# Kernel optimization log

Measured on AMD Instinct MI355X. Metric: run time of the kernel, lower is better.

The kernel has to match this reference:

```python
import jax, jax.numpy as jnp
import numpy as np

B = 8192          # batch (parallel RL envs)
LATENT = 32       # latent_size
CIN = 128         # original input_size (obs dim), c features
HID = 256         # hidden_size
ACT = 16          # num_actions
E = 8             # num_experts
GH = 128          # gate hidden size (hardcoded in module)
IN0 = LATENT + CIN    # layer-0 input dim (160)
INTER = HID + LATENT  # layer-1/2 input dim (288)
LN_EPS = 1e-5


def setup_inputs() -> dict:
    key = jax.random.key(0)
    ks = jax.random.split(key, 10)
    s = lambda k, shape, scale=1.0: jax.random.normal(k, shape, jnp.float32) * scale
    return {
        "z": s(ks[0], (B, LATENT)),
        "c": s(ks[1], (B, CIN)),
        # expert MLP params (kaiming-like small uniform scale stand-in)
        "w0": s(ks[2], (E, IN0, HID), 0.05),   "b0": jnp.full((E, HID), 0.01, jnp.float32),
        "w1": s(ks[3], (E, INTER, HID), 0.05), "b1": jnp.full((E, HID), 0.01, jnp.float32),
        "w2": s(ks[4], (E, INTER, ACT), 0.05), "b2": jnp.full((E, ACT), 0.01, jnp.float32),
        # gate MLP params
        "g0w": s(ks[5], (IN0, GH), 0.05), "g0b": jnp.zeros((GH,), jnp.float32),
        "g1w": s(ks[6], (GH, GH), 0.05),  "g1b": jnp.zeros((GH,), jnp.float32),
        "g2w": s(ks[7], (GH, E), 0.05),   "g2b": jnp.zeros((E,), jnp.float32),
        # LayerNorm on c
        "ln_g": jnp.ones((CIN,), jnp.float32),
        "ln_b": jnp.zeros((CIN,), jnp.float32),
    }


def _layer_norm(x, g, b):
    m = x.mean(-1, keepdims=True)
    v = ((x - m) ** 2).mean(-1, keepdims=True)
    return (x - m) / jnp.sqrt(v + LN_EPS) * g + b


def reference(z, c, w0, b0, w1, b1, w2, b2, g0w, g0b, g1w, g1b, g2w, g2b, ln_g, ln_b):
    cn = _layer_norm(c, ln_g, ln_b)                      # [B, CIN]
    x = jnp.concatenate([z, cn], axis=1)                 # [B, IN0]
    # gate: Linear-ELU-Linear-ELU-Linear, softmax over experts
    h = jax.nn.elu(x @ g0w + g0b)
    h = jax.nn.elu(h @ g1w + g1b)
    coeff = jax.nn.softmax(h @ g2w + g2b, axis=1)        # [B, E]

    layer_out = cn
    for w, b, act in ((w0, b0, True), (w1, b1, True), (w2, b2, False)):
        inp = jnp.concatenate([z, layer_out], axis=1)    # [B, in_dim]
        # per-expert GEMM then soft-mix (same math as coeff-mixed weight @ input)
        per = jnp.einsum('bi,eio->beo', inp, w)          # [B, E, out_dim]
        out = jnp.einsum('be,beo->bo', coeff, per) + coeff @ b  # [B, out_dim]
        layer_out = jax.nn.elu(out) if act else out
    return layer_out
```

## Files before the change

kernel.cpp:

```cpp
#include <hip/hip_runtime.h>
#include <math.h>

#define B_     8192
#define LATENT 32
#define CIN    128
#define HID    256
#define ACTD   16
#define NE     8
#define GH     128
#define IN0    160
#define INTER  288

typedef __attribute__((ext_vector_type(8))) _Float16 half8;
typedef __attribute__((ext_vector_type(4))) float    f32x4;
typedef __attribute__((ext_vector_type(4))) int      i32x4;

__device__ __forceinline__ float elu1(float x) { return x > 0.0f ? x : expm1f(x); }

__device__ __forceinline__ void gload16(const void* g, const char* lds) {
    __builtin_amdgcn_global_load_lds((const __attribute__((address_space(1))) void*)g,
                                     (__attribute__((address_space(3))) void*)lds, 16, 0, 0);
}
__device__ __forceinline__ half8 as_h8(i32x4 v) {
    union U { i32x4 a; half8 b; } u; u.a = v; return u.b;
}

__global__ __launch_bounds__(256) void k_prep_g(
    const float* __restrict__ w0, const float* __restrict__ w1, const float* __restrict__ w2,
    const float* __restrict__ g0w, const float* __restrict__ g1w,
    _Float16* __restrict__ T0, _Float16* __restrict__ T1, _Float16* __restrict__ T2,
    _Float16* __restrict__ G0, _Float16* __restrict__ G1)
{
    int g = blockIdx.x * 256 + threadIdx.x;
    const float* src; int stride; size_t dst; _Float16* H;
    if (g < 40960) {
        int e = g / 5120, r = g % 5120, o = r / 20, i0 = (r % 20) * 8;
        src = w0 + ((size_t)e * 160 + i0) * 256 + o; stride = 256;
        dst = ((size_t)e * 256 + o) * 160 + i0; H = T0;
    } else if (g < 114688) {
        int t = g - 40960;
        int e = t / 9216, r = t % 9216, o = r / 36, i0 = (r % 36) * 8;
        src = w1 + ((size_t)e * 288 + i0) * 256 + o; stride = 256;
        dst = ((size_t)e * 256 + o) * 288 + i0; H = T1;
    } else if (g < 119296) {
        int t = g - 114688;
        int e = t / 576, r = t % 576, o = r / 36, i0 = (r % 36) * 8;
        src = w2 + ((size_t)e * 288 + i0) * 16 + o; stride = 16;
        dst = ((size_t)e * 16 + o) * 288 + i0; H = T2;
    } else if (g < 121856) {
        int t = g - 119296;
        int o = t / 20, i0 = (t % 20) * 8;
        src = g0w + (size_t)i0 * 128 + o; stride = 128;
        dst = (size_t)o * 160 + i0; H = G0;
    } else if (g < 123904) {
        int t = g - 121856;
        int o = t / 16, i0 = (t % 16) * 8;
        src = g1w + (size_t)i0 * 128 + o; stride = 128;
        dst = (size_t)o * 128 + i0; H = G1;
    } else return;
    _Float16 hh[8];
    #pragma unroll
    for (int j = 0; j < 8; ++j) hh[j] = (_Float16)src[(size_t)j * stride];
    *(half8*)&H[dst] = *(const half8*)hh;
}

__global__ __launch_bounds__(256) void k_ln_concat2(
    const float* __restrict__ z, const float* __restrict__ c,
    const float* __restrict__ g, const float* __restrict__ bt,
    _Float16* __restrict__ X0, _Float16* __restrict__ X1, _Float16* __restrict__ X2)
{
    int gid = blockIdx.x * 256 + threadIdx.x;
    int row = gid >> 6;
    int l = threadIdx.x & 63;
    if (row >= B_) return;
    const float* cr = c + (size_t)row * CIN;
    float v0 = cr[l], v1 = cr[l + 64];
    float s = v0 + v1;
    #pragma unroll
    for (int o = 32; o; o >>= 1) s += __shfl_xor(s, o);
    float mean = s * (1.0f / 128.0f);
    float d0 = v0 - mean, d1 = v1 - mean;
    float q = d0 * d0 + d1 * d1;
    #pragma unroll
    for (int o = 32; o; o >>= 1) q += __shfl_xor(q, o);
    float rstd = rsqrtf(q * (1.0f / 128.0f) + 1e-5f);
    float y0 = d0 * rstd * g[l] + bt[l];
    float y1 = d1 * rstd * g[l + 64] + bt[l + 64];
    size_t r0 = (size_t)row * IN0;
    X0[r0 + 32 + l] = (_Float16)y0;
    X0[r0 + 96 + l] = (_Float16)y1;
    if (l < LATENT) {
        _Float16 zv = (_Float16)z[(size_t)row * LATENT + l];
        X0[r0 + l] = zv;
        size_t r1 = (size_t)row * INTER;
        X1[r1 + l] = zv;
        X2[r1 + l] = zv;
    }
}

__global__ __launch_bounds__(128, 2) void k_gate_fused(
    const _Float16* __restrict__ X0, const _Float16* __restrict__ G0T,
    const _Float16* __restrict__ G1T,
    const float* __restrict__ g0b, const float* __restrict__ g1b,
    const float* __restrict__ g2w, const float* __restrict__ g2b,
    float* __restrict__ coeff)
{
    __shared__ __align__(16) char smem[53248];
    const int tid = threadIdx.x, wid = tid >> 6, l = tid & 63;
    const int brow = blockIdx.x * 32;
    const int rl16 = wid * 16;

    float* wt_t = (float*)(smem + 49152);

    const int swz = (((l & 3) ^ ((l >> 3) & 3)) << 3);
    const int rq  = l >> 2;
    const int rdo = ((l & 15) << 6) + (((l >> 4) ^ ((l >> 1) & 3)) << 4);

    #pragma unroll
    for (int p = 0; p < 40; ++p) {
        if ((p & 1) != wid) continue;
        const int ks = p / 8, gg = p % 8;
        gload16(G0T + (size_t)(gg * 16 + rq) * IN0 + ks * 32 + swz, smem + p * 1024);
    }
    const _Float16* Ar0 = X0 + (size_t)(brow + rl16 + (l & 15)) * IN0 + (l >> 4) * 8;
    i32x4 a0[5];
    #pragma unroll
    for (int ks = 0; ks < 5; ++ks) a0[ks] = *(const i32x4*)(Ar0 + ks * 32);
    __syncthreads();

    f32x4 acc[8];
    #pragma unroll
    for (int nf = 0; nf < 8; ++nf) {
        float bv = g0b[nf * 16 + (l & 15)];
        acc[nf] = (f32x4){bv, bv, bv, bv};
    }
    #pragma unroll
    for (int ks = 0; ks < 5; ++ks)
        #pragma unroll
        for (int nf = 0; nf < 8; ++nf) {
            half8 b = *(const half8*)(smem + (size_t)(ks * 8 + nf) * 1024 + rdo);
            acc[nf] = __builtin_amdgcn_mfma_f32_16x16x32_f16(as_h8(a0[ks]), b, acc[nf], 0, 0, 0);
        }

    char* h1 = smem + 40960;
    #pragma unroll
    for (int nf = 0; nf < 8; ++nf)
        #pragma unroll
        for (int r = 0; r < 4; ++r) {
            const int rloc = ((l >> 4) << 2) + r;
            const int row = rl16 + rloc;
            const int colb = (nf * 16 + (l & 15)) * 2;
            *(_Float16*)(h1 + row * 256 + (colb ^ ((rloc & 7) << 4))) = (_Float16)elu1(acc[nf][r]);
        }
    __syncthreads();

    #pragma unroll
    for (int p = 0; p < 32; ++p) {
        if ((p & 1) != wid) continue;
        const int ks = p / 8, gg = p % 8;
        gload16(G1T + (size_t)(gg * 16 + rq) * GH + ks * 32 + swz, smem + p * 1024);
    }
    for (int idx = tid; idx < 1024; idx += 128)
        wt_t[(idx & 7) * 128 + (idx >> 3)] = g2w[(idx >> 3) * 8 + (idx & 7)];
    i32x4 a1[4];
    #pragma unroll
    for (int ks = 0; ks < 4; ++ks) {
        const int row = rl16 + (l & 15);
        const int off = (ks * 64 + ((l >> 4) << 4)) ^ ((row & 7) << 4);
        a1[ks] = *(const i32x4*)(h1 + row * 256 + off);
    }
    __syncthreads();

    #pragma unroll
    for (int nf = 0; nf < 8; ++nf) {
        float bv = g1b[nf * 16 + (l & 15)];
        acc[nf] = (f32x4){bv, bv, bv, bv};
    }
    #pragma unroll
    for (int ks = 0; ks < 4; ++ks)
        #pragma unroll
        for (int nf = 0; nf < 8; ++nf) {
            half8 b = *(const half8*)(smem + (size_t)(ks * 8 + nf) * 1024 + rdo);
            acc[nf] = __builtin_amdgcn_mfma_f32_16x16x32_f16(as_h8(a1[ks]), b, acc[nf], 0, 0, 0);
        }

    float pe[8][4];
    #pragma unroll
    for (int e = 0; e < 8; ++e)
        #pragma unroll
        for (int r = 0; r < 4; ++r) pe[e][r] = 0.f;
    #pragma unroll
    for (int nf = 0; nf < 8; ++nf) {
        float w_[8];
        #pragma unroll
        for (int e = 0; e < 8; ++e) w_[e] = wt_t[e * 128 + nf * 16 + (l & 15)];
        #pragma unroll
        for (int r = 0; r < 4; ++r) {
            float hv = elu1(acc[nf][r]);
            #pragma unroll
            for (int e = 0; e < 8; ++e) pe[e][r] = fmaf(hv, w_[e], pe[e][r]);
        }
    }
    #pragma unroll
    for (int off = 1; off < 16; off <<= 1)
        #pragma unroll
        for (int e = 0; e < 8; ++e)
            #pragma unroll
            for (int r = 0; r < 4; ++r) pe[e][r] += __shfl_xor(pe[e][r], off);

    if ((l & 15) == 0) {
        #pragma unroll
        for (int r = 0; r < 4; ++r) {
            float pv[8];
            float mx = -1e30f;
            #pragma unroll
            for (int e = 0; e < 8; ++e) { pv[e] = pe[e][r] + g2b[e]; mx = fmaxf(mx, pv[e]); }
            float s = 0.f;
            #pragma unroll
            for (int e = 0; e < 8; ++e) { pv[e] = expf(pv[e] - mx); s += pv[e]; }
            float inv = 1.0f / s;
            const int row = brow + rl16 + ((l >> 4) << 2) + r;
            #pragma unroll
            for (int e = 0; e < 8; ++e) coeff[(size_t)row * 8 + e] = pv[e] * inv;
        }
    }
}

template<int KS>
__global__ __launch_bounds__(256, 3) void k_moe_epar(
    const _Float16* __restrict__ A, const _Float16* __restrict__ Bw,
    const float* __restrict__ bias,
    const float* __restrict__ coeff,
    _Float16* __restrict__ outX)
{
    constexpr int K = KS * 32;
    __shared__ __align__(16) char smem[43008];

    const int tid = threadIdx.x, wid = tid >> 6, l = tid & 63;
    const int brow = (blockIdx.x >> 3) * 64;
    const int bn   = (blockIdx.x & 7) * 32;

    float* cfl = (float*)(smem + 40960);
    if (tid < 128) {
        f32x4 v = *(const f32x4*)&coeff[(size_t)(brow + (tid >> 1)) * 8 + (tid & 1) * 4];
        *(f32x4*)&cfl[tid * 4] = v;
    }

    const int swz = (((l & 3) ^ ((l >> 3) & 3)) << 3);
    const int rq  = l >> 2;
    const _Float16* sA = A + (size_t)(brow + wid * 16 + rq) * K + swz;
    const _Float16* sB2[2][2];
    #pragma unroll
    for (int e2 = 0; e2 < 2; ++e2)
        #pragma unroll
        for (int gg = 0; gg < 2; ++gg)
            sB2[e2][gg] = Bw + (size_t)((2 * wid + e2) * HID + bn + gg * 16 + rq) * K + swz;

    auto stage = [&](int bi, int k0) {
        char* buf = smem + bi * 20480;
        gload16(sA + k0, buf + wid * 1024);
        #pragma unroll
        for (int e2 = 0; e2 < 2; ++e2)
            #pragma unroll
            for (int gg = 0; gg < 2; ++gg)
                gload16(sB2[e2][gg] + k0,
                        buf + 4096 + (2 * wid + e2) * 2048 + gg * 1024);
    };

    const int rdo = ((l & 15) << 6) + (((l >> 4) ^ ((l >> 1) & 3)) << 4);
    f32x4 acc[2][4][2];
    #pragma unroll
    for (int e2 = 0; e2 < 2; ++e2)
        #pragma unroll
        for (int mf = 0; mf < 4; ++mf)
            #pragma unroll
            for (int nf = 0; nf < 2; ++nf) acc[e2][mf][nf] = (f32x4){0.f, 0.f, 0.f, 0.f};

    stage(0, 0);
    if (KS > 1) stage(1, 32);
    __syncthreads();

    for (int t = 0; t < KS; ++t) {
        const char* buf = smem + (t & 1) * 20480;
        half8 af[4];
        #pragma unroll
        for (int mf = 0; mf < 4; ++mf)
            af[mf] = *(const half8*)(buf + mf * 1024 + rdo);
        __builtin_amdgcn_s_setprio(1);
        #pragma unroll
        for (int e2 = 0; e2 < 2; ++e2) {
            const char* be = buf + 4096 + (2 * wid + e2) * 2048;
            half8 b0 = *(const half8*)(be + rdo);
            half8 b1 = *(const half8*)(be + 1024 + rdo);
            #pragma unroll
            for (int mf = 0; mf < 4; ++mf) {
                acc[e2][mf][0] = __builtin_amdgcn_mfma_f32_16x16x32_f16(af[mf], b0, acc[e2][mf][0], 0, 0, 0);
                acc[e2][mf][1] = __builtin_amdgcn_mfma_f32_16x16x32_f16(af[mf], b1, acc[e2][mf][1], 0, 0, 0);
            }
        }
        __builtin_amdgcn_s_setprio(0);
        asm volatile("s_waitcnt lgkmcnt(0)" ::: "memory");
        __builtin_amdgcn_sched_barrier(0);
        __builtin_amdgcn_s_barrier();
        if (t + 2 < KS) stage(t & 1, (t + 2) * 32);
        if (t + 1 < KS) {
            if (t + 2 < KS) { asm volatile("s_waitcnt vmcnt(5)" ::: "memory"); }
            else            { asm volatile("s_waitcnt vmcnt(0)" ::: "memory"); }
            __builtin_amdgcn_s_barrier();
            __builtin_amdgcn_sched_barrier(0);
        }
    }

    const int e0 = 2 * wid, e1 = 2 * wid + 1;
    float bv0[2], bv1[2];
    #pragma unroll
    for (int nf = 0; nf < 2; ++nf) {
        bv0[nf] = bias[e0 * HID + bn + nf * 16 + (l & 15)];
        bv1[nf] = bias[e1 * HID + bn + nf * 16 + (l & 15)];
    }
    float* red = (float*)smem;
    #pragma unroll
    for (int mf = 0; mf < 4; ++mf) {
        const int rb = mf * 16 + ((l >> 4) << 2);
        #pragma unroll
        for (int r = 0; r < 4; ++r) {
            float c0 = cfl[(rb + r) * 8 + e0];
            float c1 = cfl[(rb + r) * 8 + e1];
            #pragma unroll
            for (int nf = 0; nf < 2; ++nf) {
                float s = (acc[0][mf][nf][r] + bv0[nf]) * c0
                        + (acc[1][mf][nf][r] + bv1[nf]) * c1;
                red[wid * 2304 + (rb + r) * 36 + nf * 16 + (l & 15)] = s;
            }
        }
    }
    __syncthreads();

    const int row = tid >> 2, c0_ = (tid & 3) * 8;
    f32x4 s0 = {0.f, 0.f, 0.f, 0.f}, s1 = {0.f, 0.f, 0.f, 0.f};
    #pragma unroll
    for (int w = 0; w < 4; ++w) {
        s0 += *(const f32x4*)&red[w * 2304 + row * 36 + c0_];
        s1 += *(const f32x4*)&red[w * 2304 + row * 36 + c0_ + 4];
    }
    _Float16 hh[8];
    #pragma unroll
    for (int j = 0; j < 4; ++j) {
        hh[j]     = (_Float16)elu1(s0[j]);
        hh[4 + j] = (_Float16)elu1(s1[j]);
    }
    size_t o = (size_t)(brow + row) * INTER + 32 + bn + c0_;
    *(half8*)&outX[o] = *(const half8*)hh;
}

__global__ __launch_bounds__(128, 2) void k_final(
    const _Float16* __restrict__ X2, const _Float16* __restrict__ T2,
    const float* __restrict__ b2, const float* __restrict__ cf,
    float* __restrict__ out)
{
    __shared__ __align__(16) char smem[73728];
    const int tid = threadIdx.x, wid = tid >> 6, l = tid & 63;
    const int brow = blockIdx.x * 32;

    const int swz = (((l & 3) ^ ((l >> 3) & 3)) << 3);
    const int rq  = l >> 2;
    #pragma unroll
    for (int p = 0; p < 72; ++p) {
        if ((p & 1) != wid) continue;
        const int ks = p / 8, gg = p % 8;
        gload16(T2 + (size_t)(gg * 16 + rq) * INTER + ks * 32 + swz, smem + p * 1024);
    }
    const _Float16* Ar = X2 + (size_t)(brow + wid * 16 + (l & 15)) * INTER + (l >> 4) * 8;
    i32x4 a_[9];
    #pragma unroll
    for (int ks = 0; ks < 9; ++ks) a_[ks] = *(const i32x4*)(Ar + ks * 32);
    __syncthreads();

    const int rdo = ((l & 15) << 6) + (((l >> 4) ^ ((l >> 1) & 3)) << 4);
    f32x4 acc[8];
    #pragma unroll
    for (int nf = 0; nf < 8; ++nf) {
        float bv = b2[nf * 16 + (l & 15)];
        acc[nf] = (f32x4){bv, bv, bv, bv};
    }
    #pragma unroll
    for (int ks = 0; ks < 9; ++ks)
        #pragma unroll
        for (int nf = 0; nf < 8; ++nf) {
            half8 b = *(const half8*)(smem + (size_t)(ks * 8 + nf) * 1024 + rdo);
            acc[nf] = __builtin_amdgcn_mfma_f32_16x16x32_f16(as_h8(a_[ks]), b, acc[nf], 0, 0, 0);
        }

    #pragma unroll
    for (int r = 0; r < 4; ++r) {
        const int row = brow + wid * 16 + ((l >> 4) << 2) + r;
        const float* cr = cf + (size_t)row * 8;
        float s = 0.f;
        #pragma unroll
        for (int e = 0; e < 8; ++e) s = fmaf(cr[e], acc[e][r], s);
        out[(size_t)row * ACTD + (l & 15)] = s;
    }
}

extern "C" void kernel_launch(void* const* d_in, const int* in_sizes, int n_in,
                              void* d_out, int out_size, void* d_ws, size_t ws_size,
                              hipStream_t stream)
{
    (void)in_sizes; (void)n_in; (void)out_size; (void)ws_size;
    const float* z   = (const float*)d_in[0];
    const float* c   = (const float*)d_in[1];
    const float* w0  = (const float*)d_in[2];
    const float* b0  = (const float*)d_in[3];
    const float* w1  = (const float*)d_in[4];
    const float* b1  = (const float*)d_in[5];
    const float* w2  = (const float*)d_in[6];
    const float* b2  = (const float*)d_in[7];
    const float* g0w = (const float*)d_in[8];
    const float* g0b = (const float*)d_in[9];
    const float* g1w = (const float*)d_in[10];
    const float* g1b = (const float*)d_in[11];
    const float* g2w = (const float*)d_in[12];
    const float* g2b = (const float*)d_in[13];
    const float* lng = (const float*)d_in[14];
    const float* lnb = (const float*)d_in[15];
    float* out = (float*)d_out;

    char* p = (char*)d_ws;
    auto alloc = [&](size_t n) { char* r = p; p += (n + 255) & ~(size_t)255; return r; };
    _Float16* X0  = (_Float16*)alloc((size_t)B_ * IN0 * 2);
    _Float16* X1  = (_Float16*)alloc((size_t)B_ * INTER * 2);
    _Float16* X2  = (_Float16*)alloc((size_t)B_ * INTER * 2);
    float* cf  = (float*)alloc((size_t)B_ * NE * 4);
    _Float16* T0  = (_Float16*)alloc((size_t)NE * IN0 * HID * 2);
    _Float16* T1  = (_Float16*)alloc((size_t)NE * INTER * HID * 2);
    _Float16* T2  = (_Float16*)alloc((size_t)NE * INTER * ACTD * 2);
    _Float16* G0T = (_Float16*)alloc((size_t)IN0 * GH * 2);
    _Float16* G1T = (_Float16*)alloc((size_t)GH * GH * 2);

    k_prep_g<<<dim3(484), dim3(256), 0, stream>>>(w0, w1, w2, g0w, g1w,
        T0, T1, T2, G0T, G1T);
    k_ln_concat2<<<dim3(B_ / 4), dim3(256), 0, stream>>>(z, c, lng, lnb, X0, X1, X2);

    k_gate_fused<<<dim3(256), dim3(128), 0, stream>>>(
        X0, G0T, G1T, g0b, g1b, g2w, g2b, cf);

    k_moe_epar<5><<<dim3(1024), dim3(256), 0, stream>>>(X0, T0, b0, cf, X1);
    k_moe_epar<9><<<dim3(1024), dim3(256), 0, stream>>>(X1, T1, b1, cf, X2);

    k_final<<<dim3(256), dim3(128), 0, stream>>>(X2, T2, b2, cf, out);
}
```

Measured before the change: 68.10 us.

## Merge prep and LN kernels, prefetch gate weights, pipeline final-layer loads

Merges the weight-transpose kernel and the LayerNorm/concat kernel into one launch, saving a kernel launch and letting the two independent jobs run side by side. The gate kernel now prefetches the G1 weights and g2w into a larger LDS allocation at the start, which removes a barrier and the mid-kernel load stall. The MoE kernel swaps its block-index mapping so that consecutive blocks share the same weight column tile rather than the same rows. The final kernel issues the activation loads first, then waits on the async LDS loads one K-slice at a time with vmcnt counters, so the MFMA work overlaps the loads. The larger gate LDS footprint may reduce occupancy, and the hand-written vmcnt counts depend on the exact number of loads the compiler emits.

```diff
diff --git a/kernel.cpp b/kernel.cpp
--- a/kernel.cpp
+++ b/kernel.cpp
@@ -25,54 +25,52 @@
     union U { i32x4 a; half8 b; } u; u.a = v; return u.b;
 }
 
-__global__ __launch_bounds__(256) void k_prep_g(
+__global__ __launch_bounds__(256) void k_prep_ln(
     const float* __restrict__ w0, const float* __restrict__ w1, const float* __restrict__ w2,
     const float* __restrict__ g0w, const float* __restrict__ g1w,
-    _Float16* __restrict__ T0, _Float16* __restrict__ T1, _Float16* __restrict__ T2,
-    _Float16* __restrict__ G0, _Float16* __restrict__ G1)
-{
-    int g = blockIdx.x * 256 + threadIdx.x;
-    const float* src; int stride; size_t dst; _Float16* H;
-    if (g < 40960) {
-        int e = g / 5120, r = g % 5120, o = r / 20, i0 = (r % 20) * 8;
-        src = w0 + ((size_t)e * 160 + i0) * 256 + o; stride = 256;
-        dst = ((size_t)e * 256 + o) * 160 + i0; H = T0;
-    } else if (g < 114688) {
-        int t = g - 40960;
-        int e = t / 9216, r = t % 9216, o = r / 36, i0 = (r % 36) * 8;
-        src = w1 + ((size_t)e * 288 + i0) * 256 + o; stride = 256;
-        dst = ((size_t)e * 256 + o) * 288 + i0; H = T1;
-    } else if (g < 119296) {
-        int t = g - 114688;
-        int e = t / 576, r = t % 576, o = r / 36, i0 = (r % 36) * 8;
-        src = w2 + ((size_t)e * 288 + i0) * 16 + o; stride = 16;
-        dst = ((size_t)e * 16 + o) * 288 + i0; H = T2;
-    } else if (g < 121856) {
-        int t = g - 119296;
-        int o = t / 20, i0 = (t % 20) * 8;
-        src = g0w + (size_t)i0 * 128 + o; stride = 128;
-        dst = (size_t)o * 160 + i0; H = G0;
-    } else if (g < 123904) {
-        int t = g - 121856;
-        int o = t / 16, i0 = (t % 16) * 8;
-        src = g1w + (size_t)i0 * 128 + o; stride = 128;
-        dst = (size_t)o * 128 + i0; H = G1;
-    } else return;
-    _Float16 hh[8];
-    #pragma unroll
-    for (int j = 0; j < 8; ++j) hh[j] = (_Float16)src[(size_t)j * stride];
-    *(half8*)&H[dst] = *(const half8*)hh;
-}
-
-__global__ __launch_bounds__(256) void k_ln_concat2(
     const float* __restrict__ z, const float* __restrict__ c,
     const float* __restrict__ g, const float* __restrict__ bt,
+    _Float16* __restrict__ T0, _Float16* __restrict__ T1, _Float16* __restrict__ T2,
+    _Float16* __restrict__ G0, _Float16* __restrict__ G1,
     _Float16* __restrict__ X0, _Float16* __restrict__ X1, _Float16* __restrict__ X2)
 {
-    int gid = blockIdx.x * 256 + threadIdx.x;
+    if (blockIdx.x < 484) {
+        int gq = blockIdx.x * 256 + threadIdx.x;
+        const float* src; int stride; size_t dst; _Float16* H;
+        if (gq < 40960) {
+            int e = gq / 5120, r = gq % 5120, o = r / 20, i0 = (r % 20) * 8;
+            src = w0 + ((size_t)e * 160 + i0) * 256 + o; stride = 256;
+            dst = ((size_t)e * 256 + o) * 160 + i0; H = T0;
+        } else if (gq < 114688) {
+            int t = gq - 40960;
+            int e = t / 9216, r = t % 9216, o = r / 36, i0 = (r % 36) * 8;
+            src = w1 + ((size_t)e * 288 + i0) * 256 + o; stride = 256;
+            dst = ((size_t)e * 256 + o) * 288 + i0; H = T1;
+        } else if (gq < 119296) {
+            int t = gq - 114688;
+            int e = t / 576, r = t % 576, o = r / 36, i0 = (r % 36) * 8;
+            src = w2 + ((size_t)e * 288 + i0) * 16 + o; stride = 16;
+            dst = ((size_t)e * 16 + o) * 288 + i0; H = T2;
+        } else if (gq < 121856) {
+            int t = gq - 119296;
+            int o = t / 20, i0 = (t % 20) * 8;
+            src = g0w + (size_t)i0 * 128 + o; stride = 128;
+            dst = (size_t)o * 160 + i0; H = G0;
+        } else if (gq < 123904) {
+            int t = gq - 121856;
+            int o = t / 16, i0 = (t % 16) * 8;
+            src = g1w + (size_t)i0 * 128 + o; stride = 128;
+            dst = (size_t)o * 128 + i0; H = G1;
+        } else return;
+        _Float16 hh[8];
+        #pragma unroll
+        for (int j = 0; j < 8; ++j) hh[j] = (_Float16)src[(size_t)j * stride];
+        *(half8*)&H[dst] = *(const half8*)hh;
+        return;
+    }
+    int gid = (blockIdx.x - 484) * 256 + threadIdx.x;
     int row = gid >> 6;
     int l = threadIdx.x & 63;
-    if (row >= B_) return;
     const float* cr = c + (size_t)row * CIN;
     float v0 = cr[l], v1 = cr[l + 64];
     float s = v0 + v1;
@@ -105,12 +103,14 @@
     const float* __restrict__ g2w, const float* __restrict__ g2b,
     float* __restrict__ coeff)
 {
-    __shared__ __align__(16) char smem[53248];
+    __shared__ __align__(16) char smem[86016];
     const int tid = threadIdx.x, wid = tid >> 6, l = tid & 63;
     const int brow = blockIdx.x * 32;
     const int rl16 = wid * 16;
 
-    float* wt_t = (float*)(smem + 49152);
+    char* sG1  = smem + 40960;
+    char* h1   = smem + 73728;
+    float* wt_t = (float*)(smem + 81920);
 
     const int swz = (((l & 3) ^ ((l >> 3) & 3)) << 3);
     const int rq  = l >> 2;
@@ -122,10 +122,18 @@
         const int ks = p / 8, gg = p % 8;
         gload16(G0T + (size_t)(gg * 16 + rq) * IN0 + ks * 32 + swz, smem + p * 1024);
     }
+    #pragma unroll
+    for (int p = 0; p < 32; ++p) {
+        if ((p & 1) != wid) continue;
+        const int ks = p / 8, gg = p % 8;
+        gload16(G1T + (size_t)(gg * 16 + rq) * GH + ks * 32 + swz, sG1 + p * 1024);
+    }
     const _Float16* Ar0 = X0 + (size_t)(brow + rl16 + (l & 15)) * IN0 + (l >> 4) * 8;
     i32x4 a0[5];
     #pragma unroll
     for (int ks = 0; ks < 5; ++ks) a0[ks] = *(const i32x4*)(Ar0 + ks * 32);
+    for (int idx = tid; idx < 1024; idx += 128)
+        wt_t[(idx & 7) * 128 + (idx >> 3)] = g2w[(idx >> 3) * 8 + (idx & 7)];
     __syncthreads();
 
     f32x4 acc[8];
@@ -142,7 +150,6 @@
             acc[nf] = __builtin_amdgcn_mfma_f32_16x16x32_f16(as_h8(a0[ks]), b, acc[nf], 0, 0, 0);
         }
 
-    char* h1 = smem + 40960;
     #pragma unroll
     for (int nf = 0; nf < 8; ++nf)
         #pragma unroll
@@ -154,14 +161,6 @@
         }
     __syncthreads();
 
-    #pragma unroll
-    for (int p = 0; p < 32; ++p) {
-        if ((p & 1) != wid) continue;
-        const int ks = p / 8, gg = p % 8;
-        gload16(G1T + (size_t)(gg * 16 + rq) * GH + ks * 32 + swz, smem + p * 1024);
-    }
-    for (int idx = tid; idx < 1024; idx += 128)
-        wt_t[(idx & 7) * 128 + (idx >> 3)] = g2w[(idx >> 3) * 8 + (idx & 7)];
     i32x4 a1[4];
     #pragma unroll
     for (int ks = 0; ks < 4; ++ks) {
@@ -169,7 +168,6 @@
         const int off = (ks * 64 + ((l >> 4) << 4)) ^ ((row & 7) << 4);
         a1[ks] = *(const i32x4*)(h1 + row * 256 + off);
     }
-    __syncthreads();
 
     #pragma unroll
     for (int nf = 0; nf < 8; ++nf) {
@@ -180,7 +178,7 @@
     for (int ks = 0; ks < 4; ++ks)
         #pragma unroll
         for (int nf = 0; nf < 8; ++nf) {
-            half8 b = *(const half8*)(smem + (size_t)(ks * 8 + nf) * 1024 + rdo);
+            half8 b = *(const half8*)(sG1 + (size_t)(ks * 8 + nf) * 1024 + rdo);
             acc[nf] = __builtin_amdgcn_mfma_f32_16x16x32_f16(as_h8(a1[ks]), b, acc[nf], 0, 0, 0);
         }
 
@@ -237,8 +235,8 @@
     __shared__ __align__(16) char smem[43008];
 
     const int tid = threadIdx.x, wid = tid >> 6, l = tid & 63;
-    const int brow = (blockIdx.x >> 3) * 64;
-    const int bn   = (blockIdx.x & 7) * 32;
+    const int brow = (blockIdx.x & 127) * 64;
+    const int bn   = (blockIdx.x >> 7) * 32;
 
     float* cfl = (float*)(smem + 40960);
     if (tid < 128) {
@@ -362,6 +360,11 @@
     const int tid = threadIdx.x, wid = tid >> 6, l = tid & 63;
     const int brow = blockIdx.x * 32;
 
+    const _Float16* Ar = X2 + (size_t)(brow + wid * 16 + (l & 15)) * INTER + (l >> 4) * 8;
+    i32x4 a_[9];
+    #pragma unroll
+    for (int ks = 0; ks < 9; ++ks) a_[ks] = *(const i32x4*)(Ar + ks * 32);
+
     const int swz = (((l & 3) ^ ((l >> 3) & 3)) << 3);
     const int rq  = l >> 2;
     #pragma unroll
@@ -370,11 +373,6 @@
         const int ks = p / 8, gg = p % 8;
         gload16(T2 + (size_t)(gg * 16 + rq) * INTER + ks * 32 + swz, smem + p * 1024);
     }
-    const _Float16* Ar = X2 + (size_t)(brow + wid * 16 + (l & 15)) * INTER + (l >> 4) * 8;
-    i32x4 a_[9];
-    #pragma unroll
-    for (int ks = 0; ks < 9; ++ks) a_[ks] = *(const i32x4*)(Ar + ks * 32);
-    __syncthreads();
 
     const int rdo = ((l & 15) << 6) + (((l >> 4) ^ ((l >> 1) & 3)) << 4);
     f32x4 acc[8];
@@ -384,12 +382,30 @@
         acc[nf] = (f32x4){bv, bv, bv, bv};
     }
     #pragma unroll
-    for (int ks = 0; ks < 9; ++ks)
+    for (int ks = 0; ks < 9; ++ks) {
+        switch (ks) {
+            case 0: asm volatile("s_waitcnt vmcnt(32)" ::: "memory"); break;
+            case 1: asm volatile("s_waitcnt vmcnt(28)" ::: "memory"); break;
+            case 2: asm volatile("s_waitcnt vmcnt(24)" ::: "memory"); break;
+            case 3: asm volatile("s_waitcnt vmcnt(20)" ::: "memory"); break;
+            case 4: asm volatile("s_waitcnt vmcnt(16)" ::: "memory"); break;
+            case 5: asm volatile("s_waitcnt vmcnt(12)" ::: "memory"); break;
+            case 6: asm volatile("s_waitcnt vmcnt(8)"  ::: "memory"); break;
+            case 7: asm volatile("s_waitcnt vmcnt(4)"  ::: "memory"); break;
+            default: asm volatile("s_waitcnt vmcnt(0)" ::: "memory"); break;
+        }
+        __builtin_amdgcn_s_barrier();
+        __builtin_amdgcn_sched_barrier(0);
+        if (ks == 0) {
+            #pragma unroll
+            for (int k2 = 0; k2 < 9; ++k2) asm volatile("" : "+v"(a_[k2]));
+        }
         #pragma unroll
         for (int nf = 0; nf < 8; ++nf) {
             half8 b = *(const half8*)(smem + (size_t)(ks * 8 + nf) * 1024 + rdo);
             acc[nf] = __builtin_amdgcn_mfma_f32_16x16x32_f16(as_h8(a_[ks]), b, acc[nf], 0, 0, 0);
         }
+    }
 
     #pragma unroll
     for (int r = 0; r < 4; ++r) {
@@ -437,9 +453,9 @@
     _Float16* G0T = (_Float16*)alloc((size_t)IN0 * GH * 2);
     _Float16* G1T = (_Float16*)alloc((size_t)GH * GH * 2);
 
-    k_prep_g<<<dim3(484), dim3(256), 0, stream>>>(w0, w1, w2, g0w, g1w,
-        T0, T1, T2, G0T, G1T);
-    k_ln_concat2<<<dim3(B_ / 4), dim3(256), 0, stream>>>(z, c, lng, lnb, X0, X1, X2);
+    k_prep_ln<<<dim3(484 + B_ / 4), dim3(256), 0, stream>>>(
+        w0, w1, w2, g0w, g1w, z, c, lng, lnb,
+        T0, T1, T2, G0T, G1T, X0, X1, X2);
 
     k_gate_fused<<<dim3(256), dim3(128), 0, stream>>>(
         X0, G0T, G1T, g0b, g1b, g2w, g2b, cf);
```

Result: faster. 64.93 us (median of 2 runs) (-4.6%).
